# Kernel optimization log

Measured on AMD Instinct MI355X. Metric: run time of the kernel, lower is better.

## Reference

```python
import jax, jax.numpy as jnp
import numpy as np

SCAD_A = 3.7
PERCENTILE_Q = 0.75
EPS = 1e-8
LAM_HAT = 0.9
PROP_STEP = 4


def setup_inputs() -> dict:
    key = jax.random.key(0)
    ks = jax.random.split(key, 4)
    N, IN, H, OUT = 4096, 512, 256, 64
    p = 32.0 / N  # avg degree ~32 (pre-symmetrization ~64 after OR, still sparse)
    u = jax.random.uniform(ks[0], (N, N))
    Au = u < p
    Asym = Au | Au.T
    eye = jnp.eye(N, dtype=bool)
    A = jnp.where(eye, 0.0, Asym.astype(jnp.float32))  # zero diagonal; add_loops adds I
    X = jax.random.normal(ks[1], (N, IN), dtype=jnp.float32)
    W1 = jax.random.normal(ks[2], (IN, H), dtype=jnp.float32) / np.sqrt(IN)
    b1 = jnp.zeros((H,), dtype=jnp.float32)
    W2 = jax.random.normal(ks[3], (H, OUT), dtype=jnp.float32) / np.sqrt(H)
    b2 = jnp.zeros((OUT,), dtype=jnp.float32)
    log_gamma_0 = jnp.asarray(np.log(3.0), dtype=jnp.float32)
    raw_decay = jnp.asarray(np.log(0.85 / 0.15), dtype=jnp.float32)
    raw_alpha_blend = jnp.asarray(0.0, dtype=jnp.float32)  # sigmoid -> 0.5 blend
    return {"A": A, "X": X, "W1": W1, "b1": b1, "W2": W2, "b2": b2,
            "log_gamma_0": log_gamma_0, "raw_decay": raw_decay,
            "raw_alpha_blend": raw_alpha_blend}


def _scad_weight(y, lam, a):
    # SCAD-derived reweighting: 1 for y<=lam, (a*lam - y)/((a-1)*y) in the middle, 0 beyond a*lam.
    y_safe = jnp.maximum(y, EPS)  # avoid inf/nan in unselected branch (forward value unchanged)
    w_mid = (a * lam - y) / ((a - 1.0) * y_safe)
    return jnp.where(y <= lam, 1.0, jnp.where(y <= a * lam, w_mid, 0.0))


def reference(A, X, W1, b1, W2, b2, log_gamma_0, raw_decay, raw_alpha_blend):
    N = A.shape[0]
    eye = jnp.eye(N, dtype=A.dtype)
    Ahat = A + eye                          # add_loops
    D = Ahat.sum(-1)                        # [N]
    D_sq = jnp.sqrt(D)[:, None]             # [N,1]
    A_tilde = Ahat / (D_sq * D_sq.T)        # sym_norm: D^{-1/2} A D^{-1/2}
    edge_mask = (Ahat > 0) & (eye == 0)     # A_bool & ~I
    has_edges = edge_mask.sum() > 0

    # MLP (eval mode: dropout inactive)
    F0 = jnp.maximum(X @ W1 + b1, 0.0) @ W2 + b2   # [N, out_dim]

    alpha = jax.nn.sigmoid(raw_alpha_blend)
    g0 = jnp.exp(log_gamma_0)
    r = jax.nn.sigmoid(raw_decay)
    lam = 1.0 / LAM_HAT - 1.0

    Fc = F0
    for k in range(PROP_STEP):
        gamma_param_k = g0 * (r ** k)
        Fn = Fc / D_sq
        nrm = jnp.linalg.norm(Fn, axis=-1, keepdims=True)
        Fu = Fn / jnp.maximum(nrm, EPS)     # F.normalize semantics
        y = jnp.clip(1.0 - Fu @ Fu.T, 0.0, 2.0)  # [N,N] cosine distance
        y = jax.lax.stop_gradient(y)        # y.detach()
        y_edges = jnp.where(edge_mask, y, jnp.nan)
        gamma_data_k = jnp.nanquantile(y_edges, PERCENTILE_Q)
        gamma_data_k = jnp.maximum(jnp.where(has_edges, gamma_data_k, 1.0), EPS)
        lam_combined = alpha * (gamma_param_k / SCAD_A) + (1.0 - alpha) * (gamma_data_k / SCAD_A)
        W = _scad_weight(y, lam_combined, SCAD_A)
        W = W * (1.0 - eye)
        W = jnp.where(jnp.isnan(W), 1.0, W)
        Q_hat = ((W * Ahat).sum(-1) / D + lam)[:, None]
        Fc = (W * A_tilde) @ Fc / Q_hat + lam * F0 / Q_hat
    return Fc
```

## Files before the change

### kernel.cpp

```cpp
#include <hip/hip_runtime.h>
#include <hip/hip_cooperative_groups.h>
#include <math.h>

namespace cg = cooperative_groups;

#define N_NODES 4096
#define IN_DIM  512
#define H_DIM   256
#define OUT_DIM 64
#define SCAD_Af 3.7f
#define EPSf    1e-8f
#define NBINS   2048
#define MAXD    256
#define KSPLIT  4

__device__ __forceinline__ float scad_w(float y, float lamc) {
    if (y <= lamc) return 1.0f;
    if (y <= SCAD_Af * lamc)
        return (SCAD_Af * lamc - y) / ((SCAD_Af - 1.0f) * fmaxf(y, EPSf));
    return 0.0f;
}

__global__ __launch_bounds__(256, 4)
void k_mega(const float* __restrict__ A,  const float* __restrict__ X,
            const float* __restrict__ W1, const float* __restrict__ b1,
            const float* __restrict__ W2, const float* __restrict__ b2,
            const float* __restrict__ lg0, const float* __restrict__ rdec,
            const float* __restrict__ ralpha,
            int* __restrict__ colIdx, int* __restrict__ rowcnt,
            float* __restrict__ D, float* __restrict__ isD,
            float* __restrict__ Fu, float* __restrict__ part,
            float* __restrict__ F0, float* __restrict__ FcA,
            float* __restrict__ FcB, float* __restrict__ outp,
            unsigned int* __restrict__ hist01, float* __restrict__ y_e) {
    cg::grid_group grid = cg::this_grid();
    const int tid = threadIdx.x;
    const int blk = blockIdx.x;
    const int gid = blk * 256 + tid;
    const int w = tid >> 6, lane = tid & 63;

    __shared__ union {
        struct { float As[16][68]; float Bs[16][64]; } g;
        unsigned int hl[NBINS];
        unsigned int psum[256];
        float sh_h[4][H_DIM];
    } sm;
    __shared__ float vv[2];
    __shared__ float sh_scal;
    __shared__ int   sh_nE;
    __shared__ int   cnt4[4];

    {
        int i = blk * 4 + w;
        if (lane == 0) cnt4[w] = 0;
        __syncthreads();
        const float4* row4 = (const float4*)(A + (size_t)i * N_NODES);
        int* ci = colIdx + i * MAXD;
        for (int v = lane; v < N_NODES / 4; v += 64) {
            float4 x = row4[v];
            int j0 = v * 4;
            if (x.x != 0.0f) { int p = atomicAdd(&cnt4[w], 1); ci[p] = j0; }
            if (x.y != 0.0f) { int p = atomicAdd(&cnt4[w], 1); ci[p] = j0 + 1; }
            if (x.z != 0.0f) { int p = atomicAdd(&cnt4[w], 1); ci[p] = j0 + 2; }
            if (x.w != 0.0f) { int p = atomicAdd(&cnt4[w], 1); ci[p] = j0 + 3; }
        }
        __syncthreads();
        if (lane == 0) {
            int t = cnt4[w];
            rowcnt[i] = t;
            float d = (float)t + 1.0f;
            D[i] = d;
            isD[i] = 1.0f / sqrtf(d);
        }
        if (gid < 2 * NBINS) hist01[gid] = 0u;
        __syncthreads();
    }
    {
        int bx = blk & 3, by = (blk >> 2) & 63, bz = blk >> 8;
        int tx = tid & 15, ty = tid >> 4;
        int bm = by * 64, bn = bx * 64;
        int kbeg = bz * (IN_DIM / KSPLIT);
        float acc[4][4] = {};
        for (int k0 = kbeg; k0 < kbeg + IN_DIM / KSPLIT; k0 += 16) {
            {
                int r = tid >> 2, kv = tid & 3;
                float4 v = *(const float4*)(X + (size_t)(bm + r) * IN_DIM + k0 + kv * 4);
                sm.g.As[kv * 4 + 0][r] = v.x;
                sm.g.As[kv * 4 + 1][r] = v.y;
                sm.g.As[kv * 4 + 2][r] = v.z;
                sm.g.As[kv * 4 + 3][r] = v.w;
            }
            {
                int kk = tid >> 4, nv = tid & 15;
                *(float4*)&sm.g.Bs[kk][nv * 4] =
                    *(const float4*)(W1 + (size_t)(k0 + kk) * H_DIM + bn + nv * 4);
            }
            __syncthreads();
#pragma unroll
            for (int kk = 0; kk < 16; kk++) {
                float a[4], b[4];
#pragma unroll
                for (int u = 0; u < 4; u++) { a[u] = sm.g.As[kk][ty * 4 + u]; b[u] = sm.g.Bs[kk][tx * 4 + u]; }
#pragma unroll
                for (int u = 0; u < 4; u++)
#pragma unroll
                    for (int v = 0; v < 4; v++) acc[u][v] += a[u] * b[v];
            }
            __syncthreads();
        }
        float* Cm = part + (size_t)bz * N_NODES * H_DIM;
#pragma unroll
        for (int u = 0; u < 4; u++) {
            int m = bm + ty * 4 + u;
#pragma unroll
            for (int v = 0; v < 4; v++)
                Cm[(size_t)m * H_DIM + bn + tx * 4 + v] = acc[u][v];
        }
    }
    grid.sync();

    {
        unsigned int s = 0;
        for (int q = tid; q < N_NODES; q += 256) s += (unsigned int)rowcnt[q];
        sm.psum[tid] = s;
        __syncthreads();
        for (int off = 128; off; off >>= 1) {
            if (tid < off) sm.psum[tid] += sm.psum[tid + off];
            __syncthreads();
        }
        if (tid == 0) sh_nE = (int)sm.psum[0];
        __syncthreads();

        int i = blk * 4 + w;
        const size_t tot = (size_t)N_NODES * H_DIM;
        const float* p0 = part + (size_t)i * H_DIM;
#pragma unroll
        for (int q = 0; q < 4; q++) {
            int k = q * 64 + lane;
            float s2 = p0[k] + p0[tot + k] + p0[2 * tot + k] + p0[3 * tot + k] + b1[k];
            sm.sh_h[w][k] = fmaxf(s2, 0.0f);
        }
        const float* W2c = W2 + lane;
        float a0 = 0, a1 = 0, a2 = 0, a3 = 0;
#pragma unroll 8
        for (int k = 0; k < H_DIM; k += 4) {
            a0 += sm.sh_h[w][k + 0] * W2c[(k + 0) * OUT_DIM];
            a1 += sm.sh_h[w][k + 1] * W2c[(k + 1) * OUT_DIM];
            a2 += sm.sh_h[w][k + 2] * W2c[(k + 2) * OUT_DIM];
            a3 += sm.sh_h[w][k + 3] * W2c[(k + 3) * OUT_DIM];
        }
        float f0 = (a0 + a1) + (a2 + a3) + b2[lane];
        F0[(size_t)i * 64 + lane] = f0;
        float fn = f0 * isD[i];
        float s2 = fn * fn;
        for (int off = 32; off; off >>= 1) s2 += __shfl_xor(s2, off, 64);
        Fu[(size_t)i * 64 + lane] = fn / fmaxf(sqrtf(s2), EPSf);
    }
    grid.sync();

    const float lam = (float)(1.0 / 0.9 - 1.0);
    const int eg = lane >> 2, el = lane & 3;
    const int i = gid >> 6, c = gid & 63;
    const float* fin = F0;
    for (int k = 0; k < 4; k++) {
        float* fout = (k == 0) ? FcA : (k == 1) ? FcB : (k == 2) ? FcA : outp;
        unsigned int* histK    = hist01 + (k & 1) * NBINS;
        unsigned int* histNext = hist01 + ((k + 1) & 1) * NBINS;

        for (int b = tid; b < NBINS; b += 256) sm.hl[b] = 0u;
        __syncthreads();
        {
            int ri = blk * 4 + w;
            int deg = rowcnt[ri];
            const float4* Fu4 = (const float4*)Fu;
            float4 fi0 = Fu4[ri * 16 + el * 4 + 0];
            float4 fi1 = Fu4[ri * 16 + el * 4 + 1];
            float4 fi2 = Fu4[ri * 16 + el * 4 + 2];
            float4 fi3 = Fu4[ri * 16 + el * 4 + 3];
            for (int base = 0; base < deg; base += 16) {
                int e = base + eg;
                bool act = e < deg;
                int j = act ? colIdx[ri * MAXD + e] : ri;
                float4 a0 = Fu4[(size_t)j * 16 + el * 4 + 0];
                float4 a1 = Fu4[(size_t)j * 16 + el * 4 + 1];
                float4 a2 = Fu4[(size_t)j * 16 + el * 4 + 2];
                float4 a3 = Fu4[(size_t)j * 16 + el * 4 + 3];
                float s = fi0.x * a0.x + fi0.y * a0.y + fi0.z * a0.z + fi0.w * a0.w
                        + fi1.x * a1.x + fi1.y * a1.y + fi1.z * a1.z + fi1.w * a1.w
                        + fi2.x * a2.x + fi2.y * a2.y + fi2.z * a2.z + fi2.w * a2.w
                        + fi3.x * a3.x + fi3.y * a3.y + fi3.z * a3.z + fi3.w * a3.w;
                s += __shfl_xor(s, 1, 64);
                s += __shfl_xor(s, 2, 64);
                if (act && el == 0) {
                    float y = 1.0f - s;
                    y = fminf(fmaxf(y, 0.0f), 2.0f);
                    y_e[ri * MAXD + e] = y;
                    int bin = (int)(y * (NBINS * 0.5f));
                    if (bin > NBINS - 1) bin = NBINS - 1;
                    atomicAdd(&sm.hl[bin], 1u);
                }
            }
        }
        __syncthreads();
        for (int b = tid; b < NBINS; b += 256) {
            unsigned int v = sm.hl[b];
            if (v) atomicAdd(&histK[b], v);
        }
        if (gid < NBINS) histNext[gid] = 0u;
        grid.sync();

        {
            unsigned int cnt[8];
            const uint4* h4 = (const uint4*)histK;
            unsigned int s = 0;
#pragma unroll
            for (int q = 0; q < 2; q++) {
                uint4 v = h4[tid * 2 + q];
                cnt[q * 4 + 0] = v.x; cnt[q * 4 + 1] = v.y;
                cnt[q * 4 + 2] = v.z; cnt[q * 4 + 3] = v.w;
                s += v.x + v.y + v.z + v.w;
            }
            sm.psum[tid] = s;
            __syncthreads();
            for (int off = 1; off < 256; off <<= 1) {
                unsigned int x = 0;
                if (tid >= off) x = sm.psum[tid - off];
                __syncthreads();
                sm.psum[tid] += x;
                __syncthreads();
            }
            int nE = sh_nE;
            double h = 0.75 * (double)(nE - 1);
            long long i0 = (long long)h;
            float frac = (float)(h - (double)i0);
            unsigned int r0 = (unsigned int)i0, r1 = (unsigned int)(i0 + 1);
            unsigned int cum = (tid == 0) ? 0u : sm.psum[tid - 1];
#pragma unroll
            for (int b = 0; b < 8; b++) {
                unsigned int cn = cnt[b];
                unsigned int lo = cum;
                cum += cn;
                if (cn) {
                    float v = ((float)(tid * 8 + b) + 0.5f) * (2.0f / (float)NBINS);
                    if (lo <= r0 && r0 < cum) vv[0] = v;
                    if (lo <= r1 && r1 < cum) vv[1] = v;
                }
            }
            __syncthreads();
            if (tid == 0) {
                float gd = vv[0] + frac * (vv[1] - vv[0]);
                gd = fmaxf(gd, EPSf);
                float alpha = 1.0f / (1.0f + expf(-ralpha[0]));
                float g0 = expf(lg0[0]);
                float r = 1.0f / (1.0f + expf(-rdec[0]));
                float gp = g0;
                for (int q = 0; q < k; q++) gp *= r;
                sh_scal = alpha * (gp / SCAD_Af) + (1.0f - alpha) * (gd / SCAD_Af);
            }
            __syncthreads();
        }
        {
            float lamc = sh_scal;
            int deg = rowcnt[i];
            float acc = 0.0f, wsum = 0.0f;
            for (int base = 0; base < deg; base += 64) {
                int m = deg - base; if (m > 64) m = 64;
                int   jl = (c < m) ? colIdx[i * MAXD + base + c] : 0;
                float yl = (c < m) ? y_e[i * MAXD + base + c] : 9.0f;
                float il = (c < m) ? isD[jl] : 0.0f;
                int tt = 0;
                for (; tt + 4 <= m; tt += 4) {
                    int j0 = __shfl(jl, tt, 64),     j1 = __shfl(jl, tt + 1, 64);
                    int j2 = __shfl(jl, tt + 2, 64), j3 = __shfl(jl, tt + 3, 64);
                    float f0 = fin[(size_t)j0 * 64 + c], f1 = fin[(size_t)j1 * 64 + c];
                    float f2 = fin[(size_t)j2 * 64 + c], f3 = fin[(size_t)j3 * 64 + c];
                    float s0 = scad_w(__shfl(yl, tt, 64),     lamc);
                    float s1 = scad_w(__shfl(yl, tt + 1, 64), lamc);
                    float s2 = scad_w(__shfl(yl, tt + 2, 64), lamc);
                    float s3 = scad_w(__shfl(yl, tt + 3, 64), lamc);
                    wsum += s0 + s1 + s2 + s3;
                    acc += s0 * __shfl(il, tt, 64) * f0 + s1 * __shfl(il, tt + 1, 64) * f1
                         + s2 * __shfl(il, tt + 2, 64) * f2 + s3 * __shfl(il, tt + 3, 64) * f3;
                }
                for (; tt < m; tt++) {
                    int   j = __shfl(jl, tt, 64);
                    float y = __shfl(yl, tt, 64);
                    float wq = scad_w(y, lamc);
                    wsum += wq;
                    acc += wq * __shfl(il, tt, 64) * fin[(size_t)j * 64 + c];
                }
            }
            float Q = wsum / D[i] + lam;
            float fo = (isD[i] * acc + lam * F0[(size_t)i * 64 + c]) / Q;
            fout[(size_t)i * 64 + c] = fo;
            float fn = fo * isD[i];
            float s2n = fn * fn;
            for (int off = 32; off; off >>= 1) s2n += __shfl_xor(s2n, off, 64);
            Fu[(size_t)i * 64 + c] = fn / fmaxf(sqrtf(s2n), EPSf);
        }
        grid.sync();
        fin = fout;
    }
}

__global__ __launch_bounds__(256)
void k_init(const float* __restrict__ A, const float* __restrict__ X,
            const float* __restrict__ W1, float* __restrict__ part,
            int* __restrict__ colIdx, int* __restrict__ rowcnt,
            float* __restrict__ D, float* __restrict__ isD,
            unsigned int* __restrict__ hist01) {
    __shared__ float As[16][68];
    __shared__ float Bs[16][64];
    __shared__ int cnt4[4];
    int tid = threadIdx.x;
    if (blockIdx.x < 1024) {
        int blk = blockIdx.x;
        int bx = blk & 3, by = (blk >> 2) & 63, bz = blk >> 8;
        int tx = tid & 15, ty = tid >> 4;
        int bm = by * 64, bn = bx * 64;
        int kbeg = bz * (IN_DIM / KSPLIT);
        float acc[4][4] = {};
        for (int k0 = kbeg; k0 < kbeg + IN_DIM / KSPLIT; k0 += 16) {
            {
                int r = tid >> 2, kv = tid & 3;
                float4 v = *(const float4*)(X + (size_t)(bm + r) * IN_DIM + k0 + kv * 4);
                As[kv * 4 + 0][r] = v.x;
                As[kv * 4 + 1][r] = v.y;
                As[kv * 4 + 2][r] = v.z;
                As[kv * 4 + 3][r] = v.w;
            }
            {
                int kk = tid >> 4, nv = tid & 15;
                *(float4*)&Bs[kk][nv * 4] =
                    *(const float4*)(W1 + (size_t)(k0 + kk) * H_DIM + bn + nv * 4);
            }
            __syncthreads();
#pragma unroll
            for (int kk = 0; kk < 16; kk++) {
                float a[4], b[4];
#pragma unroll
                for (int u = 0; u < 4; u++) { a[u] = As[kk][ty * 4 + u]; b[u] = Bs[kk][tx * 4 + u]; }
#pragma unroll
                for (int u = 0; u < 4; u++)
#pragma unroll
                    for (int v = 0; v < 4; v++) acc[u][v] += a[u] * b[v];
            }
            __syncthreads();
        }
        float* Cm = part + (size_t)bz * N_NODES * H_DIM;
#pragma unroll
        for (int u = 0; u < 4; u++) {
            int m = bm + ty * 4 + u;
#pragma unroll
            for (int v = 0; v < 4; v++)
                Cm[(size_t)m * H_DIM + bn + tx * 4 + v] = acc[u][v];
        }
    } else {
        int bb = blockIdx.x - 1024;
        int gid2 = bb * 256 + tid;
        if (gid2 < 2 * NBINS) hist01[gid2] = 0u;
        int w = tid >> 6, lane = tid & 63;
        int i = bb * 4 + w;
        if (lane == 0) cnt4[w] = 0;
        __syncthreads();
        const float4* row4 = (const float4*)(A + (size_t)i * N_NODES);
        int* ci = colIdx + i * MAXD;
        for (int v = lane; v < N_NODES / 4; v += 64) {
            float4 x = row4[v];
            int j0 = v * 4;
            if (x.x != 0.0f) { int p = atomicAdd(&cnt4[w], 1); ci[p] = j0; }
            if (x.y != 0.0f) { int p = atomicAdd(&cnt4[w], 1); ci[p] = j0 + 1; }
            if (x.z != 0.0f) { int p = atomicAdd(&cnt4[w], 1); ci[p] = j0 + 2; }
            if (x.w != 0.0f) { int p = atomicAdd(&cnt4[w], 1); ci[p] = j0 + 3; }
        }
        __syncthreads();
        if (lane == 0) {
            int t = cnt4[w];
            rowcnt[i] = t;
            float d = (float)t + 1.0f;
            D[i] = d;
            isD[i] = 1.0f / sqrtf(d);
        }
    }
}

__global__ __launch_bounds__(256)
void k_mlp2(const float* __restrict__ part, const float* __restrict__ b1,
            const float* __restrict__ W2, const float* __restrict__ b2,
            const int* __restrict__ rowcnt, const float* __restrict__ isD,
            float* __restrict__ F0, float* __restrict__ Fu, int* __restrict__ nE) {
    __shared__ float sh_h[4][H_DIM];
    int tid = threadIdx.x;
    if (blockIdx.x == 0) {
        __shared__ unsigned int ps[256];
        unsigned int s = 0;
        for (int q = tid; q < N_NODES; q += 256) s += (unsigned int)rowcnt[q];
        ps[tid] = s;
        __syncthreads();
        for (int off = 128; off; off >>= 1) {
            if (tid < off) ps[tid] += ps[tid + off];
            __syncthreads();
        }
        if (tid == 0) nE[0] = (int)ps[0];
    }
    int w = tid >> 6, lane = tid & 63;
    int i = blockIdx.x * 4 + w;
    const size_t tot = (size_t)N_NODES * H_DIM;
    const float* p0 = part + (size_t)i * H_DIM;
#pragma unroll
    for (int q = 0; q < 4; q++) {
        int k = q * 64 + lane;
        float s = p0[k] + p0[tot + k] + p0[2 * tot + k] + p0[3 * tot + k] + b1[k];
        sh_h[w][k] = fmaxf(s, 0.0f);
    }
    const float* W2c = W2 + lane;
    float a0 = 0, a1 = 0, a2 = 0, a3 = 0;
#pragma unroll 8
    for (int k = 0; k < H_DIM; k += 4) {
        a0 += sh_h[w][k + 0] * W2c[(k + 0) * OUT_DIM];
        a1 += sh_h[w][k + 1] * W2c[(k + 1) * OUT_DIM];
        a2 += sh_h[w][k + 2] * W2c[(k + 2) * OUT_DIM];
        a3 += sh_h[w][k + 3] * W2c[(k + 3) * OUT_DIM];
    }
    float f0 = (a0 + a1) + (a2 + a3) + b2[lane];
    F0[(size_t)i * 64 + lane] = f0;
    float fn = f0 * isD[i];
    float s2 = fn * fn;
    for (int off = 32; off; off >>= 1) s2 += __shfl_xor(s2, off, 64);
    Fu[(size_t)i * 64 + lane] = fn / fmaxf(sqrtf(s2), EPSf);
}

__global__ __launch_bounds__(256)
void k_edgehist(const float* __restrict__ Fu, const int* __restrict__ rowcnt,
                const int* __restrict__ colIdx, float* __restrict__ y_e,
                unsigned int* __restrict__ histK) {
    __shared__ unsigned int hl[NBINS];
    for (int b = threadIdx.x; b < NBINS; b += 256) hl[b] = 0u;
    __syncthreads();
    int gid = blockIdx.x * 256 + threadIdx.x;
    int ri = gid >> 6;
    int lane = threadIdx.x & 63;
    int eg = lane >> 2, el = lane & 3;
    int deg = rowcnt[ri];
    const float4* Fu4 = (const float4*)Fu;
    float4 fi0 = Fu4[ri * 16 + el * 4 + 0];
    float4 fi1 = Fu4[ri * 16 + el * 4 + 1];
    float4 fi2 = Fu4[ri * 16 + el * 4 + 2];
    float4 fi3 = Fu4[ri * 16 + el * 4 + 3];
    for (int base = 0; base < deg; base += 16) {
        int e = base + eg;
        bool act = e < deg;
        int j = act ? colIdx[ri * MAXD + e] : ri;
        float4 a0 = Fu4[(size_t)j * 16 + el * 4 + 0];
        float4 a1 = Fu4[(size_t)j * 16 + el * 4 + 1];
        float4 a2 = Fu4[(size_t)j * 16 + el * 4 + 2];
        float4 a3 = Fu4[(size_t)j * 16 + el * 4 + 3];
        float s = fi0.x * a0.x + fi0.y * a0.y + fi0.z * a0.z + fi0.w * a0.w
                + fi1.x * a1.x + fi1.y * a1.y + fi1.z * a1.z + fi1.w * a1.w
                + fi2.x * a2.x + fi2.y * a2.y + fi2.z * a2.z + fi2.w * a2.w
                + fi3.x * a3.x + fi3.y * a3.y + fi3.z * a3.z + fi3.w * a3.w;
        s += __shfl_xor(s, 1, 64);
        s += __shfl_xor(s, 2, 64);
        if (act && el == 0) {
            float y = 1.0f - s;
            y = fminf(fmaxf(y, 0.0f), 2.0f);
            y_e[ri * MAXD + e] = y;
            int bin = (int)(y * (NBINS * 0.5f));
            if (bin > NBINS - 1) bin = NBINS - 1;
            atomicAdd(&hl[bin], 1u);
        }
    }
    __syncthreads();
    for (int b = threadIdx.x; b < NBINS; b += 256) {
        unsigned int v = hl[b];
        if (v) atomicAdd(&histK[b], v);
    }
}

__global__ __launch_bounds__(256)
void k_propq(const unsigned int* __restrict__ histK, unsigned int* __restrict__ histNext,
             const int* __restrict__ nEp, const int* __restrict__ rowcnt,
             const int* __restrict__ colIdx, const float* __restrict__ y_e,
             const float* __restrict__ Fc, const float* __restrict__ F0,
             const float* __restrict__ D, const float* __restrict__ isD,
             const float* __restrict__ lg0, const float* __restrict__ rdec,
             const float* __restrict__ ralpha, int kiter,
             float* __restrict__ Fout, float* __restrict__ FuNext) {
    __shared__ unsigned int psum[256];
    __shared__ float vv[2];
    __shared__ float sh_scal;
    int tid = threadIdx.x;
    int gid = blockIdx.x * 256 + tid;
    if (gid < NBINS) histNext[gid] = 0u;
    {
        unsigned int cnt[8];
        const uint4* h4 = (const uint4*)histK;
        unsigned int s = 0;
#pragma unroll
        for (int q = 0; q < 2; q++) {
            uint4 v = h4[tid * 2 + q];
            cnt[q * 4 + 0] = v.x; cnt[q * 4 + 1] = v.y;
            cnt[q * 4 + 2] = v.z; cnt[q * 4 + 3] = v.w;
            s += v.x + v.y + v.z + v.w;
        }
        psum[tid] = s;
        __syncthreads();
        for (int off = 1; off < 256; off <<= 1) {
            unsigned int x = 0;
            if (tid >= off) x = psum[tid - off];
            __syncthreads();
            psum[tid] += x;
            __syncthreads();
        }
        int nE = nEp[0];
        double h = 0.75 * (double)(nE - 1);
        long long i0 = (long long)h;
        float frac = (float)(h - (double)i0);
        unsigned int r0 = (unsigned int)i0, r1 = (unsigned int)(i0 + 1);
        unsigned int cum = (tid == 0) ? 0u : psum[tid - 1];
#pragma unroll
        for (int b = 0; b < 8; b++) {
            unsigned int cn = cnt[b];
            unsigned int lo = cum;
            cum += cn;
            if (cn) {
                float v = ((float)(tid * 8 + b) + 0.5f) * (2.0f / (float)NBINS);
                if (lo <= r0 && r0 < cum) vv[0] = v;
                if (lo <= r1 && r1 < cum) vv[1] = v;
            }
        }
        __syncthreads();
        if (tid == 0) {
            float gd = vv[0] + frac * (vv[1] - vv[0]);
            gd = fmaxf(gd, EPSf);
            float alpha = 1.0f / (1.0f + expf(-ralpha[0]));
            float g0 = expf(lg0[0]);
            float r = 1.0f / (1.0f + expf(-rdec[0]));
            float gp = g0;
            for (int q = 0; q < kiter; q++) gp *= r;
            sh_scal = alpha * (gp / SCAD_Af) + (1.0f - alpha) * (gd / SCAD_Af);
        }
        __syncthreads();
    }
    float lamc = sh_scal;
    const float lam = (float)(1.0 / 0.9 - 1.0);
    int i = gid >> 6, c = gid & 63;
    int deg = rowcnt[i];
    float acc = 0.0f, wsum = 0.0f;
    for (int base = 0; base < deg; base += 64) {
        int m = deg - base; if (m > 64) m = 64;
        int   jl = (c < m) ? colIdx[i * MAXD + base + c] : 0;
        float yl = (c < m) ? y_e[i * MAXD + base + c] : 9.0f;
        float il = (c < m) ? isD[jl] : 0.0f;
        int tt = 0;
        for (; tt + 4 <= m; tt += 4) {
            int j0 = __shfl(jl, tt, 64),     j1 = __shfl(jl, tt + 1, 64);
            int j2 = __shfl(jl, tt + 2, 64), j3 = __shfl(jl, tt + 3, 64);
            float f0 = Fc[(size_t)j0 * 64 + c], f1 = Fc[(size_t)j1 * 64 + c];
            float f2 = Fc[(size_t)j2 * 64 + c], f3 = Fc[(size_t)j3 * 64 + c];
            float s0 = scad_w(__shfl(yl, tt, 64),     lamc);
            float s1 = scad_w(__shfl(yl, tt + 1, 64), lamc);
            float s2 = scad_w(__shfl(yl, tt + 2, 64), lamc);
            float s3 = scad_w(__shfl(yl, tt + 3, 64), lamc);
            wsum += s0 + s1 + s2 + s3;
            acc += s0 * __shfl(il, tt, 64) * f0 + s1 * __shfl(il, tt + 1, 64) * f1
                 + s2 * __shfl(il, tt + 2, 64) * f2 + s3 * __shfl(il, tt + 3, 64) * f3;
        }
        for (; tt < m; tt++) {
            int   j = __shfl(jl, tt, 64);
            float y = __shfl(yl, tt, 64);
            float wq = scad_w(y, lamc);
            wsum += wq;
            acc += wq * __shfl(il, tt, 64) * Fc[(size_t)j * 64 + c];
        }
    }
    float Q = wsum / D[i] + lam;
    float fo = (isD[i] * acc + lam * F0[(size_t)i * 64 + c]) / Q;
    Fout[(size_t)i * 64 + c] = fo;
    float fn = fo * isD[i];
    float s2n = fn * fn;
    for (int off = 32; off; off >>= 1) s2n += __shfl_xor(s2n, off, 64);
    FuNext[(size_t)i * 64 + c] = fn / fmaxf(sqrtf(s2n), EPSf);
}

extern "C" void kernel_launch(void* const* d_in, const int* in_sizes, int n_in,
                              void* d_out, int out_size, void* d_ws, size_t ws_size,
                              hipStream_t stream) {
    const float* A      = (const float*)d_in[0];
    const float* X      = (const float*)d_in[1];
    const float* W1     = (const float*)d_in[2];
    const float* b1     = (const float*)d_in[3];
    const float* W2     = (const float*)d_in[4];
    const float* b2     = (const float*)d_in[5];
    const float* lg0    = (const float*)d_in[6];
    const float* rdec   = (const float*)d_in[7];
    const float* ralpha = (const float*)d_in[8];
    float* outp = (float*)d_out;

    char* w = (char*)d_ws;
    size_t off = 0;
    auto carve = [&](size_t bytes) -> char* {
        char* p = w + off;
        off += (bytes + 255) & ~(size_t)255;
        return p;
    };
    int*      colIdx = (int*)carve((size_t)N_NODES * MAXD * 4);
    float*    y_e    = (float*)carve((size_t)N_NODES * MAXD * 4);
    float*    part   = (float*)carve((size_t)KSPLIT * N_NODES * H_DIM * 4);
    int*      rowcnt = (int*)carve(N_NODES * 4);
    float*    D      = (float*)carve(N_NODES * 4);
    float*    isD    = (float*)carve(N_NODES * 4);
    float*    Fu     = (float*)carve((size_t)N_NODES * 64 * 4);
    float*    F0     = (float*)carve((size_t)N_NODES * 64 * 4);
    float*    FcA    = (float*)carve((size_t)N_NODES * 64 * 4);
    float*    FcB    = (float*)carve((size_t)N_NODES * 64 * 4);
    unsigned* hist01 = (unsigned*)carve(2 * NBINS * 4);
    int*      nE     = (int*)carve(256);

    int coopAttr = 0, numCU = 0, maxPerCU = 0;
    (void)hipDeviceGetAttribute(&coopAttr, hipDeviceAttributeCooperativeLaunch, 0);
    (void)hipDeviceGetAttribute(&numCU, hipDeviceAttributeMultiprocessorCount, 0);
    (void)hipOccupancyMaxActiveBlocksPerMultiprocessor(&maxPerCU, k_mega, 256, 0);
    bool useCoop = (coopAttr != 0) && ((long)maxPerCU * (long)numCU >= 1024);

    if (useCoop) {
        void* args[] = {
            (void*)&A, (void*)&X, (void*)&W1, (void*)&b1, (void*)&W2, (void*)&b2,
            (void*)&lg0, (void*)&rdec, (void*)&ralpha,
            (void*)&colIdx, (void*)&rowcnt, (void*)&D, (void*)&isD,
            (void*)&Fu, (void*)&part, (void*)&F0,
            (void*)&FcA, (void*)&FcB, (void*)&outp, (void*)&hist01, (void*)&y_e,
        };
        hipError_t e = hipLaunchCooperativeKernel((void*)k_mega, dim3(1024), dim3(256),
                                                  args, 0, stream);
        if (e == hipSuccess) return;
        (void)hipGetLastError();
    }

    k_init<<<dim3(2048), dim3(256), 0, stream>>>(A, X, W1, part, colIdx, rowcnt, D, isD, hist01);
    k_mlp2<<<dim3(1024), dim3(256), 0, stream>>>(part, b1, W2, b2, rowcnt, isD, F0, Fu, nE);
    const float* fin = F0;
    float* fouts[4] = {FcA, FcB, FcA, outp};
    for (int k = 0; k < 4; k++) {
        unsigned* histK    = hist01 + (k & 1) * NBINS;
        unsigned* histNext = hist01 + ((k + 1) & 1) * NBINS;
        k_edgehist<<<dim3(1024), dim3(256), 0, stream>>>(Fu, rowcnt, colIdx, y_e, histK);
        k_propq<<<dim3(1024), dim3(256), 0, stream>>>(histK, histNext, nE, rowcnt, colIdx,
                                                      y_e, fin, F0, D, isD, lg0, rdec,
                                                      ralpha, k, fouts[k], Fu);
        fin = fouts[k];
    }
}
```

Measured before the change: 315.0 us.

## Overlap adjacency scan with split-K GEMM and keep edge distances in LDS

```diff
diff --git a/kernel.cpp b/kernel.cpp
--- a/kernel.cpp
+++ b/kernel.cpp
@@ -13,6 +13,7 @@
 #define NBINS   2048
 #define MAXD    256
 #define KSPLIT  4
+#define KS_MG   2
 
 __device__ __forceinline__ float scad_w(float y, float lamc) {
     if (y <= lamc) return 1.0f;
@@ -32,7 +33,7 @@
             float* __restrict__ Fu, float* __restrict__ part,
             float* __restrict__ F0, float* __restrict__ FcA,
             float* __restrict__ FcB, float* __restrict__ outp,
-            unsigned int* __restrict__ hist01, float* __restrict__ y_e) {
+            unsigned int* __restrict__ hist01) {
     cg::grid_group grid = cg::this_grid();
     const int tid = threadIdx.x;
     const int blk = blockIdx.x;
@@ -43,45 +44,22 @@
         struct { float As[16][68]; float Bs[16][64]; } g;
         unsigned int hl[NBINS];
         unsigned int psum[256];
-        float sh_h[4][H_DIM];
+        struct { float h[4][H_DIM]; float w2[64][64]; } m;
     } sm;
+    __shared__ float y_loc[4][MAXD];
     __shared__ float vv[2];
     __shared__ float sh_scal;
     __shared__ int   sh_nE;
     __shared__ int   cnt4[4];
 
-    {
-        int i = blk * 4 + w;
-        if (lane == 0) cnt4[w] = 0;
-        __syncthreads();
-        const float4* row4 = (const float4*)(A + (size_t)i * N_NODES);
-        int* ci = colIdx + i * MAXD;
-        for (int v = lane; v < N_NODES / 4; v += 64) {
-            float4 x = row4[v];
-            int j0 = v * 4;
-            if (x.x != 0.0f) { int p = atomicAdd(&cnt4[w], 1); ci[p] = j0; }
-            if (x.y != 0.0f) { int p = atomicAdd(&cnt4[w], 1); ci[p] = j0 + 1; }
-            if (x.z != 0.0f) { int p = atomicAdd(&cnt4[w], 1); ci[p] = j0 + 2; }
-            if (x.w != 0.0f) { int p = atomicAdd(&cnt4[w], 1); ci[p] = j0 + 3; }
-        }
-        __syncthreads();
-        if (lane == 0) {
-            int t = cnt4[w];
-            rowcnt[i] = t;
-            float d = (float)t + 1.0f;
-            D[i] = d;
-            isD[i] = 1.0f / sqrtf(d);
-        }
-        if (gid < 2 * NBINS) hist01[gid] = 0u;
-        __syncthreads();
-    }
-    {
-        int bx = blk & 3, by = (blk >> 2) & 63, bz = blk >> 8;
+    if (blk < 512) {
+        int bz = blk >> 8, rem = blk & 255;
+        int bx = rem & 3, by = rem >> 2;
         int tx = tid & 15, ty = tid >> 4;
         int bm = by * 64, bn = bx * 64;
-        int kbeg = bz * (IN_DIM / KSPLIT);
+        int kbeg = bz * (IN_DIM / KS_MG);
         float acc[4][4] = {};
-        for (int k0 = kbeg; k0 < kbeg + IN_DIM / KSPLIT; k0 += 16) {
+        for (int k0 = kbeg; k0 < kbeg + IN_DIM / KS_MG; k0 += 16) {
             {
                 int r = tid >> 2, kv = tid & 3;
                 float4 v = *(const float4*)(X + (size_t)(bm + r) * IN_DIM + k0 + kv * 4);
@@ -111,10 +89,36 @@
         float* Cm = part + (size_t)bz * N_NODES * H_DIM;
 #pragma unroll
         for (int u = 0; u < 4; u++) {
-            int m = bm + ty * 4 + u;
+            int m2 = bm + ty * 4 + u;
 #pragma unroll
             for (int v = 0; v < 4; v++)
-                Cm[(size_t)m * H_DIM + bn + tx * 4 + v] = acc[u][v];
+                Cm[(size_t)m2 * H_DIM + bn + tx * 4 + v] = acc[u][v];
+        }
+    } else {
+        int bb = blk - 512;
+        int gid2 = bb * 256 + tid;
+        if (gid2 < 2 * NBINS) hist01[gid2] = 0u;
+#pragma unroll
+        for (int rr = 0; rr < 2; rr++) {
+            int i = bb * 8 + rr * 4 + w;
+            if (lane == 0) cnt4[w] = 0;
+            const float4* row4 = (const float4*)(A + (size_t)i * N_NODES);
+            int* ci = colIdx + i * MAXD;
+            for (int v = lane; v < N_NODES / 4; v += 64) {
+                float4 x = row4[v];
+                int j0 = v * 4;
+                if (x.x != 0.0f) { int p = atomicAdd(&cnt4[w], 1); ci[p] = j0; }
+                if (x.y != 0.0f) { int p = atomicAdd(&cnt4[w], 1); ci[p] = j0 + 1; }
+                if (x.z != 0.0f) { int p = atomicAdd(&cnt4[w], 1); ci[p] = j0 + 2; }
+                if (x.w != 0.0f) { int p = atomicAdd(&cnt4[w], 1); ci[p] = j0 + 3; }
+            }
+            if (lane == 0) {
+                int t = cnt4[w];
+                rowcnt[i] = t;
+                float d = (float)t + 1.0f;
+                D[i] = d;
+                isD[i] = 1.0f / sqrtf(d);
+            }
         }
     }
     grid.sync();
@@ -137,17 +141,24 @@
 #pragma unroll
         for (int q = 0; q < 4; q++) {
             int k = q * 64 + lane;
-            float s2 = p0[k] + p0[tot + k] + p0[2 * tot + k] + p0[3 * tot + k] + b1[k];
-            sm.sh_h[w][k] = fmaxf(s2, 0.0f);
-        }
-        const float* W2c = W2 + lane;
+            float s2 = p0[k] + p0[tot + k] + b1[k];
+            sm.m.h[w][k] = fmaxf(s2, 0.0f);
+        }
         float a0 = 0, a1 = 0, a2 = 0, a3 = 0;
-#pragma unroll 8
-        for (int k = 0; k < H_DIM; k += 4) {
-            a0 += sm.sh_h[w][k + 0] * W2c[(k + 0) * OUT_DIM];
-            a1 += sm.sh_h[w][k + 1] * W2c[(k + 1) * OUT_DIM];
-            a2 += sm.sh_h[w][k + 2] * W2c[(k + 2) * OUT_DIM];
-            a3 += sm.sh_h[w][k + 3] * W2c[(k + 3) * OUT_DIM];
+        for (int k0 = 0; k0 < H_DIM; k0 += 64) {
+            __syncthreads();
+            const float4* src = (const float4*)(W2 + (size_t)k0 * OUT_DIM);
+#pragma unroll
+            for (int q = 0; q < 4; q++)
+                ((float4*)sm.m.w2)[q * 256 + tid] = src[q * 256 + tid];
+            __syncthreads();
+#pragma unroll 16
+            for (int kk = 0; kk < 64; kk += 4) {
+                a0 += sm.m.h[w][k0 + kk + 0] * sm.m.w2[kk + 0][lane];
+                a1 += sm.m.h[w][k0 + kk + 1] * sm.m.w2[kk + 1][lane];
+                a2 += sm.m.h[w][k0 + kk + 2] * sm.m.w2[kk + 2][lane];
+                a3 += sm.m.h[w][k0 + kk + 3] * sm.m.w2[kk + 3][lane];
+            }
         }
         float f0 = (a0 + a1) + (a2 + a3) + b2[lane];
         F0[(size_t)i * 64 + lane] = f0;
@@ -160,7 +171,7 @@
 
     const float lam = (float)(1.0 / 0.9 - 1.0);
     const int eg = lane >> 2, el = lane & 3;
-    const int i = gid >> 6, c = gid & 63;
+    const int i = blk * 4 + w, c = lane;
     const float* fin = F0;
     for (int k = 0; k < 4; k++) {
         float* fout = (k == 0) ? FcA : (k == 1) ? FcB : (k == 2) ? FcA : outp;
@@ -170,17 +181,16 @@
         for (int b = tid; b < NBINS; b += 256) sm.hl[b] = 0u;
         __syncthreads();
         {
-            int ri = blk * 4 + w;
-            int deg = rowcnt[ri];
+            int deg = rowcnt[i];
             const float4* Fu4 = (const float4*)Fu;
-            float4 fi0 = Fu4[ri * 16 + el * 4 + 0];
-            float4 fi1 = Fu4[ri * 16 + el * 4 + 1];
-            float4 fi2 = Fu4[ri * 16 + el * 4 + 2];
-            float4 fi3 = Fu4[ri * 16 + el * 4 + 3];
+            float4 fi0 = Fu4[i * 16 + el * 4 + 0];
+            float4 fi1 = Fu4[i * 16 + el * 4 + 1];
+            float4 fi2 = Fu4[i * 16 + el * 4 + 2];
+            float4 fi3 = Fu4[i * 16 + el * 4 + 3];
             for (int base = 0; base < deg; base += 16) {
                 int e = base + eg;
                 bool act = e < deg;
-                int j = act ? colIdx[ri * MAXD + e] : ri;
+                int j = act ? colIdx[i * MAXD + e] : i;
                 float4 a0 = Fu4[(size_t)j * 16 + el * 4 + 0];
                 float4 a1 = Fu4[(size_t)j * 16 + el * 4 + 1];
                 float4 a2 = Fu4[(size_t)j * 16 + el * 4 + 2];
@@ -194,7 +204,7 @@
                 if (act && el == 0) {
                     float y = 1.0f - s;
                     y = fminf(fmaxf(y, 0.0f), 2.0f);
-                    y_e[ri * MAXD + e] = y;
+                    y_loc[w][e] = y;
                     int bin = (int)(y * (NBINS * 0.5f));
                     if (bin > NBINS - 1) bin = NBINS - 1;
                     atomicAdd(&sm.hl[bin], 1u);
@@ -206,6 +216,7 @@
             unsigned int v = sm.hl[b];
             if (v) atomicAdd(&histK[b], v);
         }
+        if (tid < 4 && blk * 4 + tid < NBINS) {}
         if (gid < NBINS) histNext[gid] = 0u;
         grid.sync();
 
@@ -266,7 +277,7 @@
             for (int base = 0; base < deg; base += 64) {
                 int m = deg - base; if (m > 64) m = 64;
                 int   jl = (c < m) ? colIdx[i * MAXD + base + c] : 0;
-                float yl = (c < m) ? y_e[i * MAXD + base + c] : 9.0f;
+                float yl = (c < m) ? y_loc[w][base + c] : 9.0f;
                 float il = (c < m) ? isD[jl] : 0.0f;
                 int tt = 0;
                 for (; tt + 4 <= m; tt += 4) {
@@ -629,7 +640,7 @@
             (void*)&lg0, (void*)&rdec, (void*)&ralpha,
             (void*)&colIdx, (void*)&rowcnt, (void*)&D, (void*)&isD,
             (void*)&Fu, (void*)&part, (void*)&F0,
-            (void*)&FcA, (void*)&FcB, (void*)&outp, (void*)&hist01, (void*)&y_e,
+            (void*)&FcA, (void*)&FcB, (void*)&outp, (void*)&hist01,
         };
         hipError_t e = hipLaunchCooperativeKernel((void*)k_mega, dim3(1024), dim3(256),
                                                   args, 0, stream);
```

New measurement: 307.6 us. 2.4% less time.
